# Performance work log

Measured on AMD Instinct MI355X. Metric: run time of the kernel, lower is better.

The kernel has to match this reference:

```python
import jax, jax.numpy as jnp
import numpy as np

EPS = 1e-5

def _make_mask(rng, outdim, indim, expand_size, k=3):
    # Mirrors ExpanderConv2d mask construction (indim <= outdim branch when equal)
    m = np.zeros((outdim, indim), dtype=np.float32)
    if indim > outdim:
        for i in range(outdim):
            idx = rng.permutation(indim)[:expand_size]
            m[i, idx] = 1.0
    else:
        for i in range(indim):
            idx = rng.permutation(outdim)[:expand_size]
            m[idx, i] = 1.0
    return jnp.asarray(np.broadcast_to(m[:, :, None, None], (outdim, indim, k, k)).copy())

def _bn(x, gamma, beta, mean, var):
    # eval-mode BatchNorm2d over channel axis (NCHW)
    inv = gamma / jnp.sqrt(var + EPS)
    return x * inv[None, :, None, None] + (beta - mean * inv)[None, :, None, None]

def _conv3x3(x, w, stride=1):
    return jax.lax.conv_general_dilated(
        x, w, window_strides=(stride, stride), padding=((1, 1), (1, 1)),
        dimension_numbers=('NCHW', 'OIHW', 'NCHW'))

def setup_inputs() -> dict:
    key = jax.random.key(0)
    ks = jax.random.split(key, 4)
    C = 256
    x = jax.random.normal(ks[0], (64, C, 32, 32), dtype=jnp.float32)
    fan_out = C * 9
    std = float(np.sqrt(2.0 / fan_out))  # kaiming_normal_, mode='fan_out'
    w1 = jax.random.normal(ks[1], (C, C, 3, 3), dtype=jnp.float32) * std
    w2 = jax.random.normal(ks[2], (C, C, 3, 3), dtype=jnp.float32) * std
    rng = np.random.default_rng(0)
    mask1 = _make_mask(rng, C, C, C // 8)
    mask2 = _make_mask(rng, C, C, C // 8)
    g = jax.random.uniform(ks[3], (4 * C,), minval=0.5, maxval=1.5, dtype=jnp.float32)
    return {
        'x': x,
        'bn1_gamma': g[:C], 'bn1_beta': jnp.zeros((C,), jnp.float32),
        'bn1_mean': jnp.zeros((C,), jnp.float32), 'bn1_var': jnp.ones((C,), jnp.float32),
        'w1': w1, 'mask1': mask1,
        'bn2_gamma': g[C:2 * C], 'bn2_beta': jnp.zeros((C,), jnp.float32),
        'bn2_mean': jnp.zeros((C,), jnp.float32), 'bn2_var': jnp.ones((C,), jnp.float32),
        'w2': w2, 'mask2': mask2,
    }

def reference(x, bn1_gamma, bn1_beta, bn1_mean, bn1_var, w1, mask1,
              bn2_gamma, bn2_beta, bn2_mean, bn2_var, w2, mask2):
    out = jax.nn.relu(_bn(x, bn1_gamma, bn1_beta, bn1_mean, bn1_var))
    out = _conv3x3(out, w1 * mask1)          # masked expander conv, dropout(p=0)=identity
    out = jax.nn.relu(_bn(out, bn2_gamma, bn2_beta, bn2_mean, bn2_var))
    out = _conv3x3(out, w2 * mask2, stride=1)
    return out + x                            # identity shortcut (stride=1, in==out)
```

## Files before the change

### kernel.cpp

```cpp
#include <hip/hip_runtime.h>
#include <hip/hip_bf16.h>
#include <stdint.h>

typedef __bf16 bf16_t;
typedef __bf16 bf16x8 __attribute__((ext_vector_type(8)));
typedef __bf16 bf16x4 __attribute__((ext_vector_type(4)));
typedef float  f32x4  __attribute__((ext_vector_type(4)));

#define AS_GLOBAL __attribute__((address_space(1)))
#define AS_LDS    __attribute__((address_space(3)))
#define VMW(N) asm volatile("s_waitcnt vmcnt(" #N ")" ::: "memory")

static constexpr int CCH   = 256;
static constexpr int HP    = 34;
static constexpr int PLANE = HP * HP;

__global__ void prep_params_k(const float* g1, const float* b1, const float* m1, const float* v1,
                              const float* g2, const float* b2, const float* m2, const float* v2,
                              float* prm) {
  int i = threadIdx.x;
  float i1 = g1[i] * rsqrtf(v1[i] + 1e-5f);
  prm[i]       = i1;
  prm[256 + i] = b1[i] - m1[i] * i1;
  float i2 = g2[i] * rsqrtf(v2[i] + 1e-5f);
  prm[512 + i] = i2;
  prm[768 + i] = b2[i] - m2[i] * i2;
}

__global__ __launch_bounds__(256) void prep_weights_k(const float* __restrict__ w,
                                                      const float* __restrict__ msk,
                                                      bf16_t* __restrict__ out) {
  int idx = blockIdx.x * 256 + threadIdx.x;
  const float* wp = w + (long)idx * 9;
  const float* mp = msk + (long)idx * 9;
#pragma unroll
  for (int khw = 0; khw < 9; ++khw)
    out[khw * 65536 + idx] = (bf16_t)(wp[khw] * mp[khw]);
}

__global__ __launch_bounds__(256) void zero_borders_k(bf16_t* __restrict__ t0p,
                                                      bf16_t* __restrict__ t1p) {
  const int bid = blockIdx.x;
  bf16_t* base = ((bid & 1) ? t1p : t0p) + (long)(bid >> 1) * PLANE * CCH;
  for (int i = threadIdx.x; i < 132 * 32; i += 256) {
    int pix = i >> 5, c16 = i & 31;
    int r, col;
    if (pix < 34)       { r = 0;           col = pix; }
    else if (pix < 68)  { r = 33;          col = pix - 34; }
    else if (pix < 100) { r = pix - 68 + 1; col = 0; }
    else                { r = pix - 100 + 1; col = 33; }
    *(f32x4*)&base[(r * HP + col) * CCH + c16 * 8] = f32x4{0.f, 0.f, 0.f, 0.f};
  }
}

__global__ __launch_bounds__(256) void prep_input_k(const float* __restrict__ x,
                                                    const float* __restrict__ prm,
                                                    bf16_t* __restrict__ t0p) {
  __shared__ __align__(16) bf16_t tile[64 * 256];
  const int tid = threadIdx.x;
  const int bid = blockIdx.x;
  const int n   = bid >> 4;
  const int p0  = (bid & 15) << 6;
  const int px    = tid & 63;
  const int cbase = tid >> 6;
  for (int r = 0; r < 64; ++r) {
    int ci = r * 4 + cbase;
    float v = x[((n * 256 + ci) << 10) + p0 + px];
    float y = fmaxf(v * prm[ci] + prm[256 + ci], 0.f);
    int byte = px * 512 + ((ci * 2) ^ ((px & 7) << 4));
    *(bf16_t*)((char*)tile + byte) = (bf16_t)y;
  }
  __syncthreads();
  for (int j = 0; j < 8; ++j) {
    int off  = j * 256 + tid;
    int pix  = off >> 5;
    int c16  = off & 31;
    int byte = pix * 512 + ((c16 * 16) ^ ((pix & 7) << 4));
    bf16x8 v = *(const bf16x8*)((char*)tile + byte);
    int p = p0 + pix;
    long gp = ((long)n * PLANE + ((p >> 5) + 1) * HP + (p & 31) + 1) * CCH + c16 * 8;
    *(bf16x8*)(t0p + gp) = v;
  }
}

template <int EPI>
__global__ __launch_bounds__(512, 2) void conv3x3_k(const bf16_t* __restrict__ inp,
                                                    const bf16_t* __restrict__ wts,
                                                    const float* __restrict__ prm,
                                                    const float* __restrict__ resid,
                                                    bf16_t* __restrict__ out_cl,
                                                    float* __restrict__ out_f) {
  __shared__ __align__(128) bf16_t As[3][8192];
  __shared__ __align__(128) bf16_t Bs[2][12288];

  const int tid  = threadIdx.x;
  const int lane = tid & 63;
  const int wid  = tid >> 6;
  const int wm   = wid >> 2;
  const int wn   = wid & 3;

  const int bid = blockIdx.x;
  const int n   = bid >> 2;
  const int hb  = (bid & 3) << 3;

  const int swz8 = (((lane & 3) ^ ((lane >> 2) & 3) ^ (lane >> 4)) << 3);
  const int l15  = lane & 15;
  const int k4   = lane >> 4;

  f32x4 acc[8][4];
#pragma unroll
  for (int i = 0; i < 8; ++i)
#pragma unroll
    for (int j = 0; j < 4; ++j) acc[i][j] = f32x4{0.f, 0.f, 0.f, 0.f};

  bf16x8 av[8], bv[4];

  auto stageA_half = [&](int abuf, int c, int t, int half) {
    const int ch  = wid * 2 + half;
    const int row = ch * 16 + (lane >> 2);
    const bf16_t* ga = wts + ((t * CCH + row) * CCH + (c << 5) + swz8);
    __builtin_amdgcn_global_load_lds((const AS_GLOBAL void*)ga,
                                     (AS_LDS void*)(&As[abuf][ch * 512]), 16, 0, 0);
  };

  auto stageB = [&](int bbuf, int c, int j) {
    const int ibase = wid * 3 + j;
    int s = (ibase << 6) + lane;
    if (s > 1359) s = 1359;
    const int r   = s / 136;
    const int rem = s - r * 136;
    const int cc  = rem >> 2;
    const int ks  = ((rem & 3) - (cc >> 1)) & 3;
    const bf16_t* gb = inp + ((n * PLANE + (hb + r) * HP + cc) * CCH + (c << 5) + (ks << 3));
    __builtin_amdgcn_global_load_lds((const AS_GLOBAL void*)gb,
                                     (AS_LDS void*)(&Bs[bbuf][ibase * 512]), 16, 0, 0);
  };

#define LDA(AB) do {                                                                \
    _Pragma("unroll") for (int mi = 0; mi < 8; ++mi)                                \
      av[mi] = *(const bf16x8*)&As[AB][((wm * 128 + mi * 16 + l15) << 5) + swz8];   \
  } while (0)

#define LDB(T, BB) do {                                                             \
    constexpr int KH = (T) / 3, KW = (T) % 3;                                       \
    _Pragma("unroll") for (int ni = 0; ni < 4; ++ni) {                              \
      const int p_    = (wn << 6) + (ni << 4) + l15;                                \
      const int cc_   = (p_ & 31) + KW;                                             \
      const int slot_ = ((p_ >> 5) + KH) * 136 + (cc_ << 2) + ((k4 + (cc_ >> 1)) & 3); \
      bv[ni] = *(const bf16x8*)&Bs[BB][slot_ << 3];                                 \
    }                                                                               \
  } while (0)

#define MFMA8(NJ) do {                                                              \
    _Pragma("unroll") for (int mi = 0; mi < 8; ++mi)                                \
      acc[mi][NJ] = __builtin_amdgcn_mfma_f32_16x16x32_bf16(av[mi], bv[NJ], acc[mi][NJ], 0, 0, 0); \
  } while (0)

#define TILE(t, CL7) do {                                                           \
    constexpr int AB  = (t) % 3;                                                    \
    constexpr int AB2 = ((t) + 2) % 3;                                              \
    const int bb = c & 1;                                                           \
                                       \
    LDA(AB); LDB(t, bb);                                                            \
    if ((CL7) && ((t) == 1 || (t) == 3 || (t) == 5)) stageB(bb ^ 1, c + 1, ((t) - 1) / 2); \
    if ((CL7) || (t) <= 6) {                                                        \
      if ((t) <= 6) stageA_half(AB2, c, (t) + 2, 0);                                \
      else          stageA_half(AB2, c + 1, (t) - 7, 0);                            \
    }                                                                               \
    __builtin_amdgcn_s_barrier();                                                   \
    asm volatile("s_waitcnt lgkmcnt(0)" ::: "memory");                              \
    __builtin_amdgcn_sched_barrier(0);                                              \
    __builtin_amdgcn_s_setprio(1); MFMA8(0); MFMA8(1); __builtin_amdgcn_s_setprio(0); \
    __builtin_amdgcn_s_barrier();                                                   \
                                   \
    if ((CL7) || (t) <= 6) {                                                        \
      if ((t) <= 6) stageA_half(AB2, c, (t) + 2, 1);                                \
      else          stageA_half(AB2, c + 1, (t) - 7, 1);                            \
    }                                                                               \
    __builtin_amdgcn_s_setprio(1); MFMA8(2); MFMA8(3); __builtin_amdgcn_s_setprio(0); \
    if ((CL7) || (t) <= 6) {                                                        \
      if ((CL7) && ((t) == 1 || (t) == 3 || (t) == 5)) { VMW(3); } else { VMW(2); } \
    } else if ((t) == 7) { VMW(0); }                                                \
    __builtin_amdgcn_s_barrier();                                                   \
  } while (0)

  stageB(0, 0, 0); stageB(0, 0, 1); stageB(0, 0, 2);
  stageA_half(0, 0, 0, 0); stageA_half(0, 0, 0, 1);
  stageA_half(1, 0, 1, 0); stageA_half(1, 0, 1, 1);
  VMW(2);
  __builtin_amdgcn_s_barrier();

  for (int c = 0; c < 7; ++c) {
    TILE(0, 1); TILE(1, 1); TILE(2, 1); TILE(3, 1); TILE(4, 1);
    TILE(5, 1); TILE(6, 1); TILE(7, 1); TILE(8, 1);
  }
  {
    const int c = 7;
    TILE(0, 0); TILE(1, 0); TILE(2, 0); TILE(3, 0); TILE(4, 0);
    TILE(5, 0); TILE(6, 0); TILE(7, 0); TILE(8, 0);
  }

#undef TILE
#undef LDA
#undef LDB
#undef MFMA8

  if (EPI == 0) {
#pragma unroll
    for (int mi = 0; mi < 8; ++mi) {
      const int co_b = wm * 128 + mi * 16 + ((lane >> 4) << 2);
      const float s0 = prm[co_b], s1 = prm[co_b + 1], s2 = prm[co_b + 2], s3 = prm[co_b + 3];
      const float t0 = prm[256 + co_b], t1 = prm[256 + co_b + 1],
                  t2 = prm[256 + co_b + 2], t3 = prm[256 + co_b + 3];
#pragma unroll
      for (int ni = 0; ni < 4; ++ni) {
        f32x4 v = acc[mi][ni];
        const int p  = (wn << 6) + (ni << 4) + l15;
        const int pr = p >> 5, pc = p & 31;
        bf16x4 pk;
        pk[0] = (bf16_t)fmaxf(v[0] * s0 + t0, 0.f);
        pk[1] = (bf16_t)fmaxf(v[1] * s1 + t1, 0.f);
        pk[2] = (bf16_t)fmaxf(v[2] * s2 + t2, 0.f);
        pk[3] = (bf16_t)fmaxf(v[3] * s3 + t3, 0.f);
        *(bf16x4*)&out_cl[(n * PLANE + (hb + pr + 1) * HP + pc + 1) * CCH + co_b] = pk;
      }
    }
  } else {
#pragma unroll
    for (int mi = 0; mi < 8; ++mi) {
      const int co_b = wm * 128 + mi * 16 + ((lane >> 4) << 2);
#pragma unroll
      for (int ni = 0; ni < 4; ++ni) {
        f32x4 v = acc[mi][ni];
        const int p  = (wn << 6) + (ni << 4) + l15;
        const int gp = ((n * CCH + co_b) << 10) + (hb << 5) + p;
        out_f[gp]        = v[0] + resid[gp];
        out_f[gp + 1024] = v[1] + resid[gp + 1024];
        out_f[gp + 2048] = v[2] + resid[gp + 2048];
        out_f[gp + 3072] = v[3] + resid[gp + 3072];
      }
    }
  }
}

extern "C" void kernel_launch(void* const* d_in, const int* in_sizes, int n_in,
                              void* d_out, int out_size, void* d_ws, size_t ws_size,
                              hipStream_t stream) {
  const float* x  = (const float*)d_in[0];
  const float* g1 = (const float*)d_in[1];
  const float* b1 = (const float*)d_in[2];
  const float* m1 = (const float*)d_in[3];
  const float* v1 = (const float*)d_in[4];
  const float* w1 = (const float*)d_in[5];
  const float* k1 = (const float*)d_in[6];
  const float* g2 = (const float*)d_in[7];
  const float* b2 = (const float*)d_in[8];
  const float* m2 = (const float*)d_in[9];
  const float* v2 = (const float*)d_in[10];
  const float* w2 = (const float*)d_in[11];
  const float* k2 = (const float*)d_in[12];

  char* ws = (char*)d_ws;
  const size_t T0P_B = (size_t)64 * PLANE * CCH * 2;
  bf16_t* t0p = (bf16_t*)ws;
  bf16_t* t1p = (bf16_t*)(ws + T0P_B);
  bf16_t* mw1 = (bf16_t*)(ws + 2 * T0P_B);
  bf16_t* mw2 = (bf16_t*)(ws + 2 * T0P_B + 1179648);
  float*  prm = (float*)(ws + 2 * T0P_B + 2 * 1179648);

  prep_params_k<<<1, 256, 0, stream>>>(g1, b1, m1, v1, g2, b2, m2, v2, prm);
  zero_borders_k<<<128, 256, 0, stream>>>(t0p, t1p);
  prep_weights_k<<<256, 256, 0, stream>>>(w1, k1, mw1);
  prep_weights_k<<<256, 256, 0, stream>>>(w2, k2, mw2);
  prep_input_k<<<1024, 256, 0, stream>>>(x, prm, t0p);

  conv3x3_k<0><<<256, 512, 0, stream>>>(t0p, mw1, prm + 512, nullptr, t1p, nullptr);
  conv3x3_k<1><<<256, 512, 0, stream>>>(t1p, mw2, nullptr, x, nullptr, (float*)d_out);
}
```

Measured before the change: 193.9 us.

## Double K-chunk to 64 channels with larger LDS tiles and XCD-aware block remap

Widens each K-chunk from 32 to 64 input channels, so A and B tiles double in size (two KF halves), and the pipeline becomes double-buffered instead of triple-buffered A. The MFMA work per tap is split into four 4x4 blocks, with A loads staged in quarters between them. Launch bounds drop to one block per CU to fit the larger LDS footprint. Block IDs are remapped so consecutive images land on the same XCD for L2 reuse. The aim is fewer barriers and chunk iterations, at the cost of occupancy.

New measurement: 266.9 us. 1.38x slower.

```diff
diff --git a/kernel.cpp b/kernel.cpp
--- a/kernel.cpp
+++ b/kernel.cpp
@@ -10,6 +10,7 @@
 #define AS_GLOBAL __attribute__((address_space(1)))
 #define AS_LDS    __attribute__((address_space(3)))
 #define VMW(N) asm volatile("s_waitcnt vmcnt(" #N ")" ::: "memory")
+#define LGKM0()  asm volatile("s_waitcnt lgkmcnt(0)" ::: "memory")
 
 static constexpr int CCH   = 256;
 static constexpr int HP    = 34;
@@ -84,14 +85,14 @@
 }
 
 template <int EPI>
-__global__ __launch_bounds__(512, 2) void conv3x3_k(const bf16_t* __restrict__ inp,
+__global__ __launch_bounds__(512, 1) void conv3x3_k(const bf16_t* __restrict__ inp,
                                                     const bf16_t* __restrict__ wts,
                                                     const float* __restrict__ prm,
                                                     const float* __restrict__ resid,
                                                     bf16_t* __restrict__ out_cl,
                                                     float* __restrict__ out_f) {
-  __shared__ __align__(128) bf16_t As[3][8192];
-  __shared__ __align__(128) bf16_t Bs[2][12288];
+  __shared__ __align__(128) bf16_t As[2][16384];
+  __shared__ __align__(128) bf16_t Bs[2][22272];
 
   const int tid  = threadIdx.x;
   const int lane = tid & 63;
@@ -100,12 +101,14 @@
   const int wn   = wid & 3;
 
   const int bid = blockIdx.x;
-  const int n   = bid >> 2;
-  const int hb  = (bid & 3) << 3;
-
-  const int swz8 = (((lane & 3) ^ ((lane >> 2) & 3) ^ (lane >> 4)) << 3);
-  const int l15  = lane & 15;
-  const int k4   = lane >> 4;
+  const int w   = ((bid & 7) << 5) + (bid >> 3);
+  const int n   = w >> 2;
+  const int hb  = (w & 3) << 3;
+
+  const int l15 = lane & 15;
+  const int k4  = lane >> 4;
+  const int qe  = k4 ^ (lane & 3) ^ ((lane >> 2) & 3);
+  const int h1  = (lane >> 1) & 1;
 
   f32x4 acc[8][4];
 #pragma unroll
@@ -113,108 +116,127 @@
 #pragma unroll
     for (int j = 0; j < 4; ++j) acc[i][j] = f32x4{0.f, 0.f, 0.f, 0.f};
 
-  bf16x8 av[8], bv[4];
-
-  auto stageA_half = [&](int abuf, int c, int t, int half) {
-    const int ch  = wid * 2 + half;
-    const int row = ch * 16 + (lane >> 2);
-    const bf16_t* ga = wts + ((t * CCH + row) * CCH + (c << 5) + swz8);
+  bf16x8 av[4], bv[4];
+
+  auto stageAq = [&](int abuf, int c1, int t1, int q) {
+    const int g   = q * 512 + tid;
+    const int co  = g >> 3;
+    const int ps  = tid & 7;
+    const int kfs = (ps >> 2) ^ ((tid >> 4) & 1);
+    const int qq  = (ps & 3) ^ ((tid >> 3) & 3) ^ (((q << 4) + (tid >> 5)) & 3);
+    const bf16_t* ga = wts + ((t1 * CCH + co) * CCH + (c1 << 6) + (kfs << 5) + (qq << 3));
     __builtin_amdgcn_global_load_lds((const AS_GLOBAL void*)ga,
-                                     (AS_LDS void*)(&As[abuf][ch * 512]), 16, 0, 0);
+                                     (AS_LDS void*)(&As[abuf][g * 8]), 16, 0, 0);
   };
 
-  auto stageB = [&](int bbuf, int c, int j) {
-    const int ibase = wid * 3 + j;
-    int s = (ibase << 6) + lane;
-    if (s > 1359) s = 1359;
-    const int r   = s / 136;
-    const int rem = s - r * 136;
+  auto stageBp = [&](int bbuf, int c1, int J) {
+    int sh = J * 512 + tid;
+    if (sh > 2719) sh = 2719;
+    const int kfh = (sh >= 1360) ? 1 : 0;
+    const int idx = sh - kfh * 1360;
+    const int r   = idx / 136;
+    const int rem = idx - r * 136;
     const int cc  = rem >> 2;
     const int ks  = ((rem & 3) - (cc >> 1)) & 3;
-    const bf16_t* gb = inp + ((n * PLANE + (hb + r) * HP + cc) * CCH + (c << 5) + (ks << 3));
+    const bf16_t* gb = inp + ((n * PLANE + (hb + r) * HP + cc) * CCH
+                              + (c1 << 6) + (kfh << 5) + (ks << 3));
     __builtin_amdgcn_global_load_lds((const AS_GLOBAL void*)gb,
-                                     (AS_LDS void*)(&Bs[bbuf][ibase * 512]), 16, 0, 0);
+                                     (AS_LDS void*)(&Bs[bbuf][sh * 8]), 16, 0, 0);
   };
 
-#define LDA(AB) do {                                                                \
-    _Pragma("unroll") for (int mi = 0; mi < 8; ++mi)                                \
-      av[mi] = *(const bf16x8*)&As[AB][((wm * 128 + mi * 16 + l15) << 5) + swz8];   \
-  } while (0)
-
-#define LDB(T, BB) do {                                                             \
-    constexpr int KH = (T) / 3, KW = (T) % 3;                                       \
-    _Pragma("unroll") for (int ni = 0; ni < 4; ++ni) {                              \
-      const int p_    = (wn << 6) + (ni << 4) + l15;                                \
-      const int cc_   = (p_ & 31) + KW;                                             \
+#define LDA(AB, MH, KF) do {                                                         \
+    _Pragma("unroll") for (int mi = 0; mi < 4; ++mi) {                               \
+      const int r_ = wm * 128 + (MH) * 64 + mi * 16 + l15;                           \
+      av[mi] = *(const bf16x8*)&As[AB][(r_ << 6) + (((KF) ^ h1) << 5) + (qe << 3)];  \
+    }                                                                                \
+  } while (0)
+
+#define LDB(BB, TAP, KF) do {                                                        \
+    constexpr int KH = (TAP) / 3, KW = (TAP) % 3;                                    \
+    _Pragma("unroll") for (int ni = 0; ni < 4; ++ni) {                               \
+      const int p_    = (wn << 6) + (ni << 4) + l15;                                 \
+      const int cc_   = (p_ & 31) + KW;                                              \
       const int slot_ = ((p_ >> 5) + KH) * 136 + (cc_ << 2) + ((k4 + (cc_ >> 1)) & 3); \
-      bv[ni] = *(const bf16x8*)&Bs[BB][slot_ << 3];                                 \
-    }                                                                               \
-  } while (0)
-
-#define MFMA8(NJ) do {                                                              \
-    _Pragma("unroll") for (int mi = 0; mi < 8; ++mi)                                \
-      acc[mi][NJ] = __builtin_amdgcn_mfma_f32_16x16x32_bf16(av[mi], bv[NJ], acc[mi][NJ], 0, 0, 0); \
-  } while (0)
-
-#define TILE(t, CL7) do {                                                           \
-    constexpr int AB  = (t) % 3;                                                    \
-    constexpr int AB2 = ((t) + 2) % 3;                                              \
-    const int bb = c & 1;                                                           \
-                                       \
-    LDA(AB); LDB(t, bb);                                                            \
-    if ((CL7) && ((t) == 1 || (t) == 3 || (t) == 5)) stageB(bb ^ 1, c + 1, ((t) - 1) / 2); \
-    if ((CL7) || (t) <= 6) {                                                        \
-      if ((t) <= 6) stageA_half(AB2, c, (t) + 2, 0);                                \
-      else          stageA_half(AB2, c + 1, (t) - 7, 0);                            \
-    }                                                                               \
-    __builtin_amdgcn_s_barrier();                                                   \
-    asm volatile("s_waitcnt lgkmcnt(0)" ::: "memory");                              \
-    __builtin_amdgcn_sched_barrier(0);                                              \
-    __builtin_amdgcn_s_setprio(1); MFMA8(0); MFMA8(1); __builtin_amdgcn_s_setprio(0); \
-    __builtin_amdgcn_s_barrier();                                                   \
-                                   \
-    if ((CL7) || (t) <= 6) {                                                        \
-      if ((t) <= 6) stageA_half(AB2, c, (t) + 2, 1);                                \
-      else          stageA_half(AB2, c + 1, (t) - 7, 1);                            \
-    }                                                                               \
-    __builtin_amdgcn_s_setprio(1); MFMA8(2); MFMA8(3); __builtin_amdgcn_s_setprio(0); \
-    if ((CL7) || (t) <= 6) {                                                        \
-      if ((CL7) && ((t) == 1 || (t) == 3 || (t) == 5)) { VMW(3); } else { VMW(2); } \
-    } else if ((t) == 7) { VMW(0); }                                                \
-    __builtin_amdgcn_s_barrier();                                                   \
-  } while (0)
-
-  stageB(0, 0, 0); stageB(0, 0, 1); stageB(0, 0, 2);
-  stageA_half(0, 0, 0, 0); stageA_half(0, 0, 0, 1);
-  stageA_half(1, 0, 1, 0); stageA_half(1, 0, 1, 1);
+      bv[ni] = *(const bf16x8*)&Bs[BB][(KF) * 10880 + slot_ * 8];                    \
+    }                                                                                \
+  } while (0)
+
+#define MFMA16(MH) do {                                                              \
+    _Pragma("unroll") for (int mi = 0; mi < 4; ++mi)                                 \
+    _Pragma("unroll") for (int ni = 0; ni < 4; ++ni)                                 \
+      acc[(MH) * 4 + mi][ni] =                                                       \
+        __builtin_amdgcn_mfma_f32_16x16x32_bf16(av[mi], bv[ni], acc[(MH)*4+mi][ni], 0, 0, 0); \
+  } while (0)
+
+#define MMA_BLK(MH) do {                                                             \
+    __builtin_amdgcn_s_barrier();                                                    \
+    LGKM0();                                                                         \
+    __builtin_amdgcn_sched_barrier(0);                                               \
+    __builtin_amdgcn_s_setprio(1); MFMA16(MH); __builtin_amdgcn_s_setprio(0);        \
+    __builtin_amdgcn_s_barrier();                                                    \
+  } while (0)
+
+#define STEP(TAP, LASTC) do {                                                        \
+    const int ab = (c + (TAP)) & 1;                                                  \
+    const int bb = c & 1;                                                            \
+    constexpr int TN = ((TAP) + 1) % 9;                                              \
+    const int cN = c + ((TAP) == 8);                                                 \
+                                                                \
+    LDA(ab, 0, 0); LDB(bb, TAP, 0);                                                  \
+    if (!((LASTC) && (TAP) == 8)) stageAq(ab ^ 1, cN, TN, 0);                        \
+    if ((TAP) >= 1 && (TAP) <= 6 && !(LASTC)) { VMW(2); }                            \
+    else if ((LASTC) && (TAP) == 8) { VMW(0); }                                      \
+    else { VMW(1); }                                                                 \
+    MMA_BLK(0);                                                                      \
+                                                                \
+    LDA(ab, 1, 0);                                                                   \
+    if (!((LASTC) && (TAP) == 8)) stageAq(ab ^ 1, cN, TN, 2);                        \
+    MMA_BLK(1);                                                                      \
+                                                                \
+    LDA(ab, 0, 1); LDB(bb, TAP, 1);                                                  \
+    if (!((LASTC) && (TAP) == 8)) stageAq(ab ^ 1, cN, TN, 1);                        \
+    MMA_BLK(0);                                                                      \
+                                                                \
+    LDA(ab, 1, 1);                                                                   \
+    if (!((LASTC) && (TAP) == 8)) stageAq(ab ^ 1, cN, TN, 3);                        \
+    if (!(LASTC) && (TAP) <= 5) stageBp(bb ^ 1, c + 1, TAP);                         \
+    if (!((LASTC) && (TAP) == 8)) {                                                  \
+      if (!(LASTC) && (TAP) <= 5) { VMW(3); } else { VMW(2); }                       \
+    }                                                                                \
+    MMA_BLK(1);                                                                      \
+  } while (0)
+
+  stageBp(0, 0, 0); stageBp(0, 0, 1); stageBp(0, 0, 2);
+  stageBp(0, 0, 3); stageBp(0, 0, 4); stageBp(0, 0, 5);
+  stageAq(0, 0, 0, 0); stageAq(0, 0, 0, 2); stageAq(0, 0, 0, 1); stageAq(0, 0, 0, 3);
   VMW(2);
   __builtin_amdgcn_s_barrier();
 
-  for (int c = 0; c < 7; ++c) {
-    TILE(0, 1); TILE(1, 1); TILE(2, 1); TILE(3, 1); TILE(4, 1);
-    TILE(5, 1); TILE(6, 1); TILE(7, 1); TILE(8, 1);
-  }
-  {
-    const int c = 7;
-    TILE(0, 0); TILE(1, 0); TILE(2, 0); TILE(3, 0); TILE(4, 0);
-    TILE(5, 0); TILE(6, 0); TILE(7, 0); TILE(8, 0);
-  }
-
-#undef TILE
+  int c = 0;
+#pragma unroll 1
+  for (; c < 3; ++c) {
+    STEP(0, 0); STEP(1, 0); STEP(2, 0); STEP(3, 0); STEP(4, 0);
+    STEP(5, 0); STEP(6, 0); STEP(7, 0); STEP(8, 0);
+  }
+  STEP(0, 1); STEP(1, 1); STEP(2, 1); STEP(3, 1); STEP(4, 1);
+  STEP(5, 1); STEP(6, 1); STEP(7, 1); STEP(8, 1);
+
+#undef STEP
+#undef MMA_BLK
+#undef MFMA16
+#undef LDB
 #undef LDA
-#undef LDB
-#undef MFMA8
 
   if (EPI == 0) {
 #pragma unroll
-    for (int mi = 0; mi < 8; ++mi) {
-      const int co_b = wm * 128 + mi * 16 + ((lane >> 4) << 2);
+    for (int m = 0; m < 8; ++m) {
+      const int co_b = wm * 128 + (m >> 2) * 64 + (m & 3) * 16 + ((lane >> 4) << 2);
       const float s0 = prm[co_b], s1 = prm[co_b + 1], s2 = prm[co_b + 2], s3 = prm[co_b + 3];
       const float t0 = prm[256 + co_b], t1 = prm[256 + co_b + 1],
                   t2 = prm[256 + co_b + 2], t3 = prm[256 + co_b + 3];
 #pragma unroll
       for (int ni = 0; ni < 4; ++ni) {
-        f32x4 v = acc[mi][ni];
+        f32x4 v = acc[m][ni];
         const int p  = (wn << 6) + (ni << 4) + l15;
         const int pr = p >> 5, pc = p & 31;
         bf16x4 pk;
@@ -227,11 +249,11 @@
     }
   } else {
 #pragma unroll
-    for (int mi = 0; mi < 8; ++mi) {
-      const int co_b = wm * 128 + mi * 16 + ((lane >> 4) << 2);
+    for (int m = 0; m < 8; ++m) {
+      const int co_b = wm * 128 + (m >> 2) * 64 + (m & 3) * 16 + ((lane >> 4) << 2);
 #pragma unroll
       for (int ni = 0; ni < 4; ++ni) {
-        f32x4 v = acc[mi][ni];
+        f32x4 v = acc[m][ni];
         const int p  = (wn << 6) + (ni << 4) + l15;
         const int gp = ((n * CCH + co_b) << 10) + (hb << 5) + p;
         out_f[gp]        = v[0] + resid[gp];
```
